# Performance work log

Measured on AMD Instinct MI355X. Metric: run time of the kernel, lower is better.

Reference implementation:

```python
import jax, jax.numpy as jnp
import numpy as np

KAPPA = 0.5


def setup_inputs() -> dict:
    key = jax.random.key(0)
    embeddings = jax.random.normal(key, (8, 4096, 64), dtype=jnp.float32)
    return {"embeddings": embeddings}


def reference(embeddings):
    # logits[b, n, m] = kappa * <emb[b,n], emb[b,m]>   -> [B, N, N]
    logits = KAPPA * jnp.einsum("bnd,bmd->bnm", embeddings, embeddings)
    B = logits.shape[0]
    # logsumexp over both matrix dims, per batch element
    loss = jax.scipy.special.logsumexp(logits.reshape(B, -1), axis=1)
    return loss.mean()
```

## Files before the change

### kernel.cpp

```cpp
#include <hip/hip_runtime.h>
#include <math.h>

#define BATCH 8
#define NTOK  4096
#define DIM   64
#define BM    128
#define NT    (NTOK / BM)
#define TPB   (NT * (NT + 1) / 2)
#define KAPPA 0.5f

typedef _Float16 f16x8 __attribute__((ext_vector_type(8)));
typedef float    f32x16 __attribute__((ext_vector_type(16)));

__global__ __launch_bounds__(256, 2)
void gram_lse_partial(const float* __restrict__ emb, float* __restrict__ ws) {
    __shared__ f16x8 As[8 * BM];
    __shared__ f16x8 Bs[8 * BM];
    __shared__ float red_m[4], red_s[4];

    const int tid = threadIdx.x;
    const int bb  = blockIdx.x;
    const int b   = bb / TPB;
    int t = bb - b * TPB;
    int ti = 0;
    while (t >= NT - ti) { t -= NT - ti; ++ti; }
    const int tj = ti + t;

    const float* embA = emb + ((size_t)b * NTOK + (size_t)ti * BM) * DIM;
    const float* embB = emb + ((size_t)b * NTOK + (size_t)tj * BM) * DIM;

    {
        const int g  = tid & 7;
        const int r0 = tid >> 3;
#pragma unroll
        for (int p = 0; p < 4; ++p) {
            const int row = r0 + 32 * p;
            const float4 a0 = *(const float4*)(embA + (size_t)row * DIM + g * 8);
            const float4 a1 = *(const float4*)(embA + (size_t)row * DIM + g * 8 + 4);
            const float4 b0 = *(const float4*)(embB + (size_t)row * DIM + g * 8);
            const float4 b1 = *(const float4*)(embB + (size_t)row * DIM + g * 8 + 4);
            f16x8 pa, pb;
            pa[0] = (_Float16)a0.x; pa[1] = (_Float16)a0.y;
            pa[2] = (_Float16)a0.z; pa[3] = (_Float16)a0.w;
            pa[4] = (_Float16)a1.x; pa[5] = (_Float16)a1.y;
            pa[6] = (_Float16)a1.z; pa[7] = (_Float16)a1.w;
            pb[0] = (_Float16)b0.x; pb[1] = (_Float16)b0.y;
            pb[2] = (_Float16)b0.z; pb[3] = (_Float16)b0.w;
            pb[4] = (_Float16)b1.x; pb[5] = (_Float16)b1.y;
            pb[6] = (_Float16)b1.z; pb[7] = (_Float16)b1.w;
            As[g * BM + (row ^ g)] = pa;
            Bs[g * BM + (row ^ g)] = pb;
        }
    }
    __syncthreads();

    const int lane = tid & 63;
    const int w    = tid >> 6;
    const int half = lane >> 5;
    const int ln31 = lane & 31;
    const int waveR = (w & 1) * 64;
    const int waveC = (w >> 1) * 64;

    f32x16 acc00 = {}, acc01 = {}, acc10 = {}, acc11 = {};
#pragma unroll
    for (int s = 0; s < 4; ++s) {
        const int g = 2 * s + half;
        const f16x8 a0 = As[g * BM + ((waveR + ln31) ^ g)];
        const f16x8 a1 = As[g * BM + ((waveR + 32 + ln31) ^ g)];
        const f16x8 b0 = Bs[g * BM + ((waveC + ln31) ^ g)];
        const f16x8 b1 = Bs[g * BM + ((waveC + 32 + ln31) ^ g)];
        acc00 = __builtin_amdgcn_mfma_f32_32x32x16_f16(a0, b0, acc00, 0, 0, 0);
        acc01 = __builtin_amdgcn_mfma_f32_32x32x16_f16(a0, b1, acc01, 0, 0, 0);
        acc10 = __builtin_amdgcn_mfma_f32_32x32x16_f16(a1, b0, acc10, 0, 0, 0);
        acc11 = __builtin_amdgcn_mfma_f32_32x32x16_f16(a1, b1, acc11, 0, 0, 0);
    }

    float lm = -INFINITY;
#pragma unroll
    for (int e = 0; e < 16; ++e) {
        lm = fmaxf(lm, acc00[e]); lm = fmaxf(lm, acc01[e]);
        lm = fmaxf(lm, acc10[e]); lm = fmaxf(lm, acc11[e]);
    }
#pragma unroll
    for (int off = 32; off > 0; off >>= 1)
        lm = fmaxf(lm, __shfl_xor(lm, off));
    if (lane == 0) red_m[w] = lm;
    __syncthreads();
    const float M = KAPPA * fmaxf(fmaxf(red_m[0], red_m[1]),
                                  fmaxf(red_m[2], red_m[3]));

    float lsum = 0.f;
#pragma unroll
    for (int e = 0; e < 16; ++e) {
        lsum += __expf(fmaf(KAPPA, acc00[e], -M));
        lsum += __expf(fmaf(KAPPA, acc01[e], -M));
        lsum += __expf(fmaf(KAPPA, acc10[e], -M));
        lsum += __expf(fmaf(KAPPA, acc11[e], -M));
    }
#pragma unroll
    for (int off = 32; off > 0; off >>= 1)
        lsum += __shfl_xor(lsum, off);
    if (lane == 0) red_s[w] = lsum;
    __syncthreads();
    if (tid == 0) {
        const float wgt = (ti == tj) ? 1.f : 2.f;
        ws[2 * (size_t)bb]     = M;
        ws[2 * (size_t)bb + 1] = wgt * (red_s[0] + red_s[1] + red_s[2] + red_s[3]);
    }
}

__global__ __launch_bounds__(512)
void reduce_lse(const float* __restrict__ ws, float* __restrict__ out) {
    const int tid  = threadIdx.x;
    const int w    = tid >> 6;
    const int lane = tid & 63;
    __shared__ float lse[BATCH];

    const float* p = ws + (size_t)w * TPB * 2;
    float mv[9], lv[9];
    int cnt = 0;
    for (int idx = lane; idx < TPB; idx += 64) {
        mv[cnt] = p[2 * idx];
        lv[cnt] = p[2 * idx + 1];
        ++cnt;
    }
    float lm = -INFINITY;
    for (int c = 0; c < cnt; ++c) lm = fmaxf(lm, mv[c]);
#pragma unroll
    for (int off = 32; off > 0; off >>= 1) lm = fmaxf(lm, __shfl_down(lm, off));
    const float L = __shfl(lm, 0);

    float s = 0.f;
    for (int c = 0; c < cnt; ++c) s += lv[c] * __expf(mv[c] - L);
#pragma unroll
    for (int off = 32; off > 0; off >>= 1) s += __shfl_down(s, off);

    if (lane == 0) lse[w] = L + logf(s);
    __syncthreads();
    if (tid == 0) {
        float a = 0.f;
        for (int i = 0; i < BATCH; ++i) a += lse[i];
        out[0] = a * (1.f / BATCH);
    }
}

extern "C" void kernel_launch(void* const* d_in, const int* in_sizes, int n_in,
                              void* d_out, int out_size, void* d_ws, size_t ws_size,
                              hipStream_t stream) {
    const float* emb = (const float*)d_in[0];
    float* out = (float*)d_out;
    float* ws  = (float*)d_ws;

    gram_lse_partial<<<BATCH * TPB, 256, 0, stream>>>(emb, ws);
    reduce_lse<<<1, 512, 0, stream>>>(ws, out);
}
```

Measured before the change: 82.40 us.

## Fuse final LSE reduction into gram kernel via last-block atomic counter

Replaces the separate reduction kernel with a last-block-done pattern: each block writes its partial, bumps a global atomic counter, and the final block reduces all partials and writes the mean. Per-wave max and sum are combined in one pass, dropping a block-wide barrier, and exp is switched to a base-2 hardware instruction with prescaled constants. Occupancy hint is raised to 3 blocks per CU. This adds a memset launch for the counter plus atomic and fence overhead, and relies on threadfence ordering for correctness.

New measurement: 185.2 us. +124.7%, slower.

```diff
diff --git a/kernel.cpp b/kernel.cpp
--- a/kernel.cpp
+++ b/kernel.cpp
@@ -7,16 +7,30 @@
 #define BM    128
 #define NT    (NTOK / BM)
 #define TPB   (NT * (NT + 1) / 2)
+#define GRID  (BATCH * TPB)
 #define KAPPA 0.5f
+#define LOG2E 1.4426950408889634f
+#define LN2   0.6931471805599453f
 
 typedef _Float16 f16x8 __attribute__((ext_vector_type(8)));
 typedef float    f32x16 __attribute__((ext_vector_type(16)));
 
-__global__ __launch_bounds__(256, 2)
-void gram_lse_partial(const float* __restrict__ emb, float* __restrict__ ws) {
+__device__ __forceinline__ float EXP2(float x) {
+#if __has_builtin(__builtin_amdgcn_exp2f)
+    return __builtin_amdgcn_exp2f(x);
+#else
+    return __expf(x * LN2);
+#endif
+}
+
+__global__ __launch_bounds__(256, 3)
+void gram_lse_fused(const float* __restrict__ emb, float* __restrict__ ws,
+                    unsigned* __restrict__ counter, float* __restrict__ out) {
     __shared__ f16x8 As[8 * BM];
     __shared__ f16x8 Bs[8 * BM];
     __shared__ float red_m[4], red_s[4];
+    __shared__ float lse8[BATCH];
+    __shared__ int   isLast;
 
     const int tid = threadIdx.x;
     const int bb  = blockIdx.x;
@@ -75,7 +89,8 @@
         acc11 = __builtin_amdgcn_mfma_f32_32x32x16_f16(a1, b1, acc11, 0, 0, 0);
     }
 
-    float lm = -INFINITY;
+    const float c2 = KAPPA * LOG2E;
+    float lm = acc00[0];
 #pragma unroll
     for (int e = 0; e < 16; ++e) {
         lm = fmaxf(lm, acc00[e]); lm = fmaxf(lm, acc01[e]);
@@ -84,62 +99,58 @@
 #pragma unroll
     for (int off = 32; off > 0; off >>= 1)
         lm = fmaxf(lm, __shfl_xor(lm, off));
-    if (lane == 0) red_m[w] = lm;
-    __syncthreads();
-    const float M = KAPPA * fmaxf(fmaxf(red_m[0], red_m[1]),
-                                  fmaxf(red_m[2], red_m[3]));
+    const float m2 = c2 * lm;
 
     float lsum = 0.f;
 #pragma unroll
     for (int e = 0; e < 16; ++e) {
-        lsum += __expf(fmaf(KAPPA, acc00[e], -M));
-        lsum += __expf(fmaf(KAPPA, acc01[e], -M));
-        lsum += __expf(fmaf(KAPPA, acc10[e], -M));
-        lsum += __expf(fmaf(KAPPA, acc11[e], -M));
+        lsum += EXP2(fmaf(c2, acc00[e], -m2));
+        lsum += EXP2(fmaf(c2, acc01[e], -m2));
+        lsum += EXP2(fmaf(c2, acc10[e], -m2));
+        lsum += EXP2(fmaf(c2, acc11[e], -m2));
     }
 #pragma unroll
     for (int off = 32; off > 0; off >>= 1)
         lsum += __shfl_xor(lsum, off);
-    if (lane == 0) red_s[w] = lsum;
+    if (lane == 0) { red_m[w] = m2; red_s[w] = lsum; }
     __syncthreads();
+
     if (tid == 0) {
+        const float M2 = fmaxf(fmaxf(red_m[0], red_m[1]),
+                               fmaxf(red_m[2], red_m[3]));
+        float S = red_s[0] * EXP2(red_m[0] - M2)
+                + red_s[1] * EXP2(red_m[1] - M2)
+                + red_s[2] * EXP2(red_m[2] - M2)
+                + red_s[3] * EXP2(red_m[3] - M2);
         const float wgt = (ti == tj) ? 1.f : 2.f;
-        ws[2 * (size_t)bb]     = M;
-        ws[2 * (size_t)bb + 1] = wgt * (red_s[0] + red_s[1] + red_s[2] + red_s[3]);
+        ws[2 * (size_t)bb]     = M2;
+        ws[2 * (size_t)bb + 1] = wgt * S;
+        __threadfence();
+        isLast = (atomicAdd(counter, 1u) == GRID - 1) ? 1 : 0;
     }
-}
+    __syncthreads();
+    if (!isLast) return;
 
-__global__ __launch_bounds__(512)
-void reduce_lse(const float* __restrict__ ws, float* __restrict__ out) {
-    const int tid  = threadIdx.x;
-    const int w    = tid >> 6;
-    const int lane = tid & 63;
-    __shared__ float lse[BATCH];
-
-    const float* p = ws + (size_t)w * TPB * 2;
-    float mv[9], lv[9];
-    int cnt = 0;
-    for (int idx = lane; idx < TPB; idx += 64) {
-        mv[cnt] = p[2 * idx];
-        lv[cnt] = p[2 * idx + 1];
-        ++cnt;
+    __threadfence();
+    for (int bq = w; bq < BATCH; bq += 4) {
+        const float* p = ws + (size_t)bq * TPB * 2;
+        float L = -INFINITY;
+        for (int idx = lane; idx < TPB; idx += 64) L = fmaxf(L, p[2 * idx]);
+#pragma unroll
+        for (int off = 32; off > 0; off >>= 1)
+            L = fmaxf(L, __shfl_xor(L, off));
+        float s = 0.f;
+        for (int idx = lane; idx < TPB; idx += 64)
+            s += p[2 * idx + 1] * EXP2(p[2 * idx] - L);
+#pragma unroll
+        for (int off = 32; off > 0; off >>= 1)
+            s += __shfl_xor(s, off);
+        if (lane == 0) lse8[bq] = LN2 * (L + log2f(s));
     }
-    float lm = -INFINITY;
-    for (int c = 0; c < cnt; ++c) lm = fmaxf(lm, mv[c]);
-#pragma unroll
-    for (int off = 32; off > 0; off >>= 1) lm = fmaxf(lm, __shfl_down(lm, off));
-    const float L = __shfl(lm, 0);
-
-    float s = 0.f;
-    for (int c = 0; c < cnt; ++c) s += lv[c] * __expf(mv[c] - L);
-#pragma unroll
-    for (int off = 32; off > 0; off >>= 1) s += __shfl_down(s, off);
-
-    if (lane == 0) lse[w] = L + logf(s);
     __syncthreads();
     if (tid == 0) {
         float a = 0.f;
-        for (int i = 0; i < BATCH; ++i) a += lse[i];
+        for (int i = 0; i < BATCH; ++i) a += lse8[i];
         out[0] = a * (1.f / BATCH);
     }
 }
@@ -150,7 +161,8 @@
     const float* emb = (const float*)d_in[0];
     float* out = (float*)d_out;
     float* ws  = (float*)d_ws;
+    unsigned* counter = (unsigned*)((char*)d_ws + 2 * (size_t)GRID * sizeof(float));
 
-    gram_lse_partial<<<BATCH * TPB, 256, 0, stream>>>(emb, ws);
-    reduce_lse<<<1, 512, 0, stream>>>(ws, out);
+    hipMemsetAsync(counter, 0, sizeof(unsigned), stream);
+    gram_lse_fused<<<GRID, 256, 0, stream>>>(emb, ws, counter, out);
 }
```
